# Optimization experiments

Hardware: AMD Instinct MI355X
Metric: run time of the kernel (lower is better)

Reference implementation:

```python
import jax, jax.numpy as jnp
import numpy as np
from math import factorial

# ---- static config (mirrors init_kwargs) ----
ZS = np.array([1, 6, 7, 8], dtype=np.int64)
NZ = 4
N_ATOM_BASIS = 3
CHAN = N_ATOM_BASIS ** 2          # 9 edge channels
MAX_L = 3
N_RBF = 8                          # radial basis functions
N_RB = 8                           # radial embedding dim
CUTOFF = 5.5
P_CUT = 6
MP_NORM = 1.0 / 10.0 ** 0.5        # 1/sqrt(avg_num_neighbors)
NUM_MP = 1
N_NODES = 4000
N_EDGES = 48000

def _make_l_list(max_l):
    lst = []
    for l in range(max_l + 1):
        for lx in range(l, -1, -1):
            for ly in range(l - lx, -1, -1):
                lst.append((lx, ly, l - lx - ly))
    return lst

L_LIST = _make_l_list(MAX_L)       # 20 (lx,ly,lz) tuples
N_L = len(L_LIST)
L_OF = np.array([sum(t) for t in L_LIST], dtype=np.int32)
LX = np.array([t[0] for t in L_LIST])
LY = np.array([t[1] for t in L_LIST])
LZ = np.array([t[2] for t in L_LIST])
# multinomial prefactors l!/(lx!ly!lz!), grouped per l for the nu=2 symmetrizer
PREF = np.array([factorial(sum(t)) / (factorial(t[0]) * factorial(t[1]) * factorial(t[2])) for t in L_LIST], dtype=np.float32)
SYM2 = np.zeros((N_L, MAX_L + 1), dtype=np.float32)
SYM2[np.arange(N_L), L_OF] = PREF

def _bessel_rbf(r):
    # r: [E,1] -> [E, N_RBF];  e_n(r) = sqrt(2/rc) * sin(n pi r / rc) / r
    n = jnp.arange(1, N_RBF + 1, dtype=r.dtype)
    return jnp.sqrt(2.0 / CUTOFF) * jnp.sin(n * jnp.pi * r / CUTOFF) / r

def _poly_cutoff(r):
    p = float(P_CUT)
    u = r / CUTOFF
    f = 1.0 - 0.5 * (p + 1.0) * (p + 2.0) * u ** p + p * (p + 2.0) * u ** (p + 1.0) - 0.5 * p * (p + 1.0) * u ** (p + 2.0)
    return f * (u < 1.0)

def _angular(unit):
    # monomials x^lx * y^ly * z^lz of the unit edge vector -> [E, N_L]
    x, y, z = unit[:, 0:1], unit[:, 1:2], unit[:, 2:3]
    return (x ** jnp.asarray(LX)) * (y ** jnp.asarray(LY)) * (z ** jnp.asarray(LZ))

def _radial_transform(A, W_rt):
    # shared per-l linear map along radial axis: [N, N_RBF, N_L, C] -> [N, N_RB, N_L, C]
    Wg = W_rt[jnp.asarray(L_OF)]   # [N_L, N_RBF, N_RB]
    return jnp.einsum('nric,irs->nsic', A, Wg)

def _symmetrize(A):
    # nu=1: A at lxlylz=(0,0,0); nu=2, each l: sum_{|lxlylz|=l} multinomial * A^2
    B1 = A[:, :, 0:1, :]
    B2 = jnp.einsum('nric,il->nrlc', A * A, jnp.asarray(SYM2))
    return jnp.concatenate([B1, B2], axis=2)   # [N, N_RB, 1+(MAX_L+1), C]

def _forward(positions, shifts, W_emb, W_rt, W_nm, atomic_numbers, edge_index):
    sender, receiver = edge_index[0], edge_index[1]
    one_hot = (atomic_numbers[:, None] == jnp.asarray(ZS)[None, :]).astype(positions.dtype)
    node_emb = one_hot @ W_emb                                    # [N, n_atom_basis]
    # edge encoding: flattened outer product of sender/receiver embeddings -> [E, CHAN]
    enc = (node_emb[sender][:, :, None] * node_emb[receiver][:, None, :]).reshape(-1, CHAN)
    vec = positions[receiver] - positions[sender] + shifts
    lengths = jnp.linalg.norm(vec, axis=-1, keepdims=True)        # [E,1]
    unit = vec / lengths
    rc = _bessel_rbf(lengths) * _poly_cutoff(lengths)             # [E, N_RBF]
    ang = _angular(unit)                                          # [E, N_L]
    edge_attri = rc[:, :, None, None] * ang[:, None, :, None] * enc[:, None, None, :]
    A = jax.ops.segment_sum(edge_attri, receiver, num_segments=N_NODES)
    A = _radial_transform(A, W_rt)                                # [N, N_RB, N_L, C]
    B = _symmetrize(A)
    feats = [B]
    Wnm_exp = W_nm[:, :, jnp.asarray(L_OF), :]                    # expand per-l memory weights to lxlylz
    for _ in range(NUM_MP):
        memory = A * Wnm_exp                                      # NodeMemory
        chi = B.sum(axis=(1, 2))                                  # [N, C] invariant scalar per channel
        msg_B = edge_attri * chi[sender][:, None, None, :]        # MesssageBchi
        A_B = _radial_transform(jax.ops.segment_sum(msg_B, receiver, num_segments=N_NODES), W_rt)
        msg_A = A[sender] * rc[:, :, None, None]                  # MessageAr: radial-weighted sender A
        A = (A_B + jax.ops.segment_sum(msg_A, receiver, num_segments=N_NODES)) * MP_NORM + memory
        B = _symmetrize(A)
        feats.append(B)
    return jnp.stack(feats, axis=-1)                              # [N, N_RB, 5, C, 1+NUM_MP]

def setup_inputs() -> dict:
    key = jax.random.key(0)
    k = jax.random.split(key, 8)
    positions = jax.random.uniform(k[0], (N_NODES, 3), dtype=jnp.float32) * 3.0
    shifts = jnp.zeros((N_EDGES, 3), dtype=jnp.float32)
    species_idx = jax.random.randint(k[1], (N_NODES,), 0, NZ)
    atomic_numbers = jnp.asarray(ZS)[species_idx]
    sender = jax.random.randint(k[2], (N_EDGES,), 0, N_NODES)
    receiver = (sender + 1 + jax.random.randint(k[3], (N_EDGES,), 0, N_NODES - 1)) % N_NODES  # no self-edges
    edge_index = jnp.stack([sender, receiver])
    W_emb = jax.random.normal(k[4], (NZ, N_ATOM_BASIS), dtype=jnp.float32) * 0.5
    W_rt = jax.random.normal(k[5], (MAX_L + 1, N_RBF, N_RB), dtype=jnp.float32) / np.sqrt(N_RBF)
    W_nm = jax.random.uniform(k[6], (1, N_RB, MAX_L + 1, CHAN), dtype=jnp.float32)
    return {"positions": positions, "shifts": shifts, "W_emb": W_emb, "W_rt": W_rt, "W_nm": W_nm, "atomic_numbers": atomic_numbers, "edge_index": edge_index}

def reference(positions, shifts, W_emb, W_rt, W_nm, atomic_numbers, edge_index):
    return _forward(positions, shifts, W_emb, W_rt, W_nm, atomic_numbers, edge_index)
```

## Files before the change

### kernel.cpp

```cpp
#include <hip/hip_runtime.h>
#include <hip/hip_fp16.h>

#ifndef M_PIf
#define M_PIf 3.14159265358979323846f
#endif

constexpr int NNODE = 4000;
constexpr int NEDGE = 48000;
constexpr int NLA   = 20;
constexpr int NCH   = 9;
constexpr int NRB   = 8;
constexpr int NEL   = NRB * NLA * NCH;
constexpr int NP2   = NEL / 2;
constexpr int FW    = 40;
constexpr int EC    = 32;
constexpr float CUT = 5.5f;
constexpr float MPN = 0.316227766016837933f;

__constant__ int   c_LOF[NLA]  = {0,1,1,1,2,2,2,2,2,2,3,3,3,3,3,3,3,3,3,3};
__constant__ float c_PREF[NLA] = {1,1,1,1,1,2,2,1,2,1,1,3,3,3,6,3,1,3,3,1};
__constant__ int   c_GB[4] = {0,0,1,4};
__constant__ int   c_GE[4] = {0,1,4,10};

__global__ void k_count(const int* __restrict__ ei, int* __restrict__ counts) {
  int e = blockIdx.x * blockDim.x + threadIdx.x;
  if (e >= NEDGE) return;
  atomicAdd(&counts[ei[NEDGE + e]], 1);
}

__global__ void k_scan(const int* __restrict__ counts, int* __restrict__ offsets,
                       int* __restrict__ cursor) {
  __shared__ int wsum[16];
  int t = threadIdx.x;
  int base = t*4;
  int c0 = (base+0 < NNODE) ? counts[base+0] : 0;
  int c1 = (base+1 < NNODE) ? counts[base+1] : 0;
  int c2 = (base+2 < NNODE) ? counts[base+2] : 0;
  int c3 = (base+3 < NNODE) ? counts[base+3] : 0;
  int s = c0+c1+c2+c3;
  int lane = t & 63, w = t >> 6;
  int incl = s;
  #pragma unroll
  for (int d = 1; d < 64; d <<= 1) {
    int v = __shfl_up(incl, d);
    if (lane >= d) incl += v;
  }
  if (lane == 63) wsum[w] = incl;
  __syncthreads();
  if (t < 16) {
    int v = wsum[t];
    int inc2 = v;
    #pragma unroll
    for (int d = 1; d < 16; d <<= 1) {
      int u = __shfl_up(inc2, d);
      if (t >= d) inc2 += u;
    }
    wsum[t] = inc2 - v;
  }
  __syncthreads();
  int excl = wsum[w] + incl - s;
  int o0 = excl, o1 = o0+c0, o2 = o1+c1, o3 = o2+c2;
  if (base+0 < NNODE) { offsets[base+0]=o0; cursor[base+0]=o0; }
  if (base+1 < NNODE) { offsets[base+1]=o1; cursor[base+1]=o1; }
  if (base+2 < NNODE) { offsets[base+2]=o2; cursor[base+2]=o2; }
  if (base+3 < NNODE) { offsets[base+3]=o3; cursor[base+3]=o3; }
  if (t == 1023) offsets[NNODE] = excl + s;
}

__global__ void k_edgec(const float* __restrict__ pos, const float* __restrict__ shifts,
                        const int* __restrict__ ei, const int* __restrict__ an,
                        const float* __restrict__ W_emb,
                        int* __restrict__ cursor, float* __restrict__ facS,
                        int* __restrict__ sndS) {
  int e = blockIdx.x * blockDim.x + threadIdx.x;
  if (e >= NEDGE) return;
  int snd = ei[e];
  int rcv = ei[NEDGE + e];
  float vx = pos[rcv*3+0] - pos[snd*3+0] + shifts[e*3+0];
  float vy = pos[rcv*3+1] - pos[snd*3+1] + shifts[e*3+1];
  float vz = pos[rcv*3+2] - pos[snd*3+2] + shifts[e*3+2];
  float len = sqrtf(vx*vx + vy*vy + vz*vz);
  float inv = 1.0f / len;
  float x = vx*inv, y = vy*inv, z = vz*inv;
  float u  = len * (1.0f/CUT);
  float u2 = u*u;
  float u6 = u2*u2*u2;
  float fcut = 1.0f - 28.0f*u6 + 48.0f*u6*u - 21.0f*u6*u2;
  if (u >= 1.0f) fcut = 0.0f;
  float pre = sqrtf(2.0f/CUT) * fcut * inv;
  int p = atomicAdd(&cursor[rcv], 1);
  float* f = facS + (size_t)p*FW;
  float s1 = __sinf(M_PIf * u);
  float cth = __cosf(M_PIf * u);
  float two_c = 2.0f * cth;
  float sm1 = 0.0f, sc = s1;
  #pragma unroll
  for (int j = 0; j < NRB; ++j) {
    f[j] = pre * sc;
    float nx = two_c * sc - sm1;
    sm1 = sc; sc = nx;
  }
  float ang[NLA];
  ang[0]=1.0f; ang[1]=x; ang[2]=y; ang[3]=z;
  ang[4]=x*x; ang[5]=x*y; ang[6]=x*z; ang[7]=y*y; ang[8]=y*z; ang[9]=z*z;
  ang[10]=ang[4]*x; ang[11]=ang[4]*y; ang[12]=ang[4]*z;
  ang[13]=x*ang[7]; ang[14]=ang[5]*z; ang[15]=x*ang[9];
  ang[16]=ang[7]*y; ang[17]=ang[7]*z; ang[18]=y*ang[9]; ang[19]=ang[9]*z;
  #pragma unroll
  for (int i = 0; i < NLA; ++i) f[8+i] = ang[i];
  int as_ = an[snd], ar_ = an[rcv];
  int sps = (as_==1)?0:(as_==6)?1:(as_==7)?2:3;
  int spr = (ar_==1)?0:(ar_==6)?1:(ar_==7)?2:3;
  float es0=W_emb[sps*3+0], es1=W_emb[sps*3+1], es2=W_emb[sps*3+2];
  float er0=W_emb[spr*3+0], er1=W_emb[spr*3+1], er2=W_emb[spr*3+2];
  f[28]=es0*er0; f[29]=es0*er1; f[30]=es0*er2;
  f[31]=es1*er0; f[32]=es1*er1; f[33]=es1*er2;
  f[34]=es2*er0; f[35]=es2*er1; f[36]=es2*er2;
  f[37]=0.f; f[38]=0.f; f[39]=0.f;
  sndS[p] = snd;
}

__global__ void k_echi(float* __restrict__ facS, const int* __restrict__ sndS,
                       const float* __restrict__ chi) {
  int p = blockIdx.x * blockDim.x + threadIdx.x;
  if (p >= NEDGE) return;
  int snd = sndS[p];
  float* f = facS + (size_t)p*FW;
  #pragma unroll
  for (int c = 0; c < 9; ++c)
    f[28 + c] = chi[snd*9 + c] * f[28 + c];
}


__global__ __launch_bounds__(256, 8) void k_nodeA(
    const float* __restrict__ facS, const int* __restrict__ offsets,
    const float* __restrict__ W_rt,
    __half2* __restrict__ A1h2,
    float* __restrict__ chi) {
  __shared__ float s_wrt[256];
  __shared__ float s_e[EC*FW];
  __shared__ float s_tile[8*90];
  __shared__ float s_B[288];
  int bid = blockIdx.x;
  int n = bid >> 1, half = bid & 1;
  int t = threadIdx.x;
  s_wrt[t] = W_rt[t];
  int rq[2], kk[2], i0[2], c0[2], l0[2], i1[2], c1[2], l1[2], qg[2];
  bool val[2];
  #pragma unroll
  for (int jj = 0; jj < 2; ++jj) {
    int j = t + jj*256;
    val[jj] = (j < 360);
    int js = val[jj] ? j : 0;
    rq[jj] = js / 45; kk[jj] = js % 45;
    qg[jj] = half*360 + js;
    int rem0 = 2*(kk[jj] + 45*half);
    i0[jj] = rem0 / 9;  c0[jj] = rem0 % 9;  l0[jj] = c_LOF[i0[jj]];
    int rem1 = rem0 + 1;
    i1[jj] = rem1 / 9;  c1[jj] = rem1 % 9;  l1[jj] = c_LOF[i1[jj]];
  }
  float acc[2][2] = {{0,0},{0,0}};
  int beg = offsets[n], end = offsets[n+1];
  const float4* f4 = (const float4*)facS;
  for (int base = beg; base < end; base += EC) {
    int m = min(EC, end - base);
    if (base != beg) __syncthreads();
    for (int idx = t; idx < m*(FW/4); idx += 256)
      ((float4*)s_e)[idx] = f4[(size_t)base*(FW/4) + idx];
    __syncthreads();
    for (int p = 0; p < m; ++p) {
      const float* e0 = s_e + p*FW;
      #pragma unroll
      for (int jj = 0; jj < 2; ++jj) {
        if (val[jj]) {
          float rv = e0[rq[jj]];
          acc[jj][0] += rv * e0[8+i0[jj]] * e0[28+c0[jj]];
          acc[jj][1] += rv * e0[8+i1[jj]] * e0[28+c1[jj]];
        }
      }
    }
  }
  __syncthreads();
  #pragma unroll
  for (int jj = 0; jj < 2; ++jj)
    if (val[jj]) {
      s_tile[rq[jj]*90 + 2*kk[jj]]     = acc[jj][0];
      s_tile[rq[jj]*90 + 2*kk[jj] + 1] = acc[jj][1];
    }
  __syncthreads();
  float a1v[2][2];
  #pragma unroll
  for (int jj = 0; jj < 2; ++jj) {
    if (val[jj]) {
      float ab0 = 0.f, ab1 = 0.f;
      #pragma unroll
      for (int r = 0; r < NRB; ++r) {
        ab0 += s_tile[r*90 + 2*kk[jj]]     * s_wrt[l0[jj]*64 + r*8 + rq[jj]];
        ab1 += s_tile[r*90 + 2*kk[jj] + 1] * s_wrt[l1[jj]*64 + r*8 + rq[jj]];
      }
      a1v[jj][0] = ab0; a1v[jj][1] = ab1;
      A1h2[(size_t)n*NP2 + qg[jj]] = __floats2half2_rn(ab0, ab1);
    }
  }
  __syncthreads();
  #pragma unroll
  for (int jj = 0; jj < 2; ++jj)
    if (val[jj]) {
      s_tile[rq[jj]*90 + 2*kk[jj]]     = a1v[jj][0];
      s_tile[rq[jj]*90 + 2*kk[jj] + 1] = a1v[jj][1];
    }
  __syncthreads();
  if (half == 0) {
    for (int m2 = t; m2 < 288; m2 += 256) {
      int s = m2 / 36, rm = m2 % 36, l5 = rm / 9, c = rm % 9;
      float b;
      if (l5 == 0) b = s_tile[s*90 + c];
      else {
        b = 0.f;
        for (int i = c_GB[l5]; i < c_GE[l5]; ++i) {
          float v = s_tile[s*90 + i*9 + c];
          b += c_PREF[i]*v*v;
        }
      }
      s_B[m2] = b;
    }
    __syncthreads();
    if (t < 9) {
      float x = 0.f;
      #pragma unroll
      for (int u = 0; u < 32; ++u) x += s_B[u*9 + t];
      atomicAdd(&chi[n*9 + t], x);
    }
  } else {
    if (t < 72) {
      int s = t / 9, c = t % 9;
      float b = 0.f;
      for (int i = 10; i < 20; ++i) {
        float v = s_tile[s*90 + (i-10)*9 + c];
        b += c_PREF[i]*v*v;
      }
      s_B[t] = b;
    }
    __syncthreads();
    if (t < 9) {
      float x = 0.f;
      #pragma unroll
      for (int u = 0; u < 8; ++u) x += s_B[u*9 + t];
      atomicAdd(&chi[n*9 + t], x);
    }
  }
}

__global__ __launch_bounds__(256, 8) void k_nodeMP(
    const float* __restrict__ facS, const int* __restrict__ offsets,
    const int* __restrict__ sndS,
    const float* __restrict__ W_rt, const float* __restrict__ W_nm,
    const __half2* __restrict__ A1h2,
    float* __restrict__ out) {
  __shared__ float s_wrt[256];
  __shared__ float s_wnm[288];
  __shared__ float s_e[EC*FW];
  __shared__ float s_tile[8*90];
  int bid = blockIdx.x;
  int n = bid >> 1, half = bid & 1;
  int t = threadIdx.x;
  s_wrt[t] = W_rt[t];
  s_wnm[t] = W_nm[t];
  if (t < 32) s_wnm[256 + t] = W_nm[256 + t];
  int rq[2], kk[2], i0[2], c0[2], l0[2], i1[2], c1[2], l1[2], qg[2];
  bool val[2];
  #pragma unroll
  for (int jj = 0; jj < 2; ++jj) {
    int j = t + jj*256;
    val[jj] = (j < 360);
    int js = val[jj] ? j : 0;
    rq[jj] = js / 45; kk[jj] = js % 45;
    qg[jj] = half*360 + js;
    int rem0 = 2*(kk[jj] + 45*half);
    i0[jj] = rem0 / 9;  c0[jj] = rem0 % 9;  l0[jj] = c_LOF[i0[jj]];
    int rem1 = rem0 + 1;
    i1[jj] = rem1 / 9;  c1[jj] = rem1 % 9;  l1[jj] = c_LOF[i1[jj]];
  }
  float accA[2][2] = {{0,0},{0,0}};
  float accB[2][2] = {{0,0},{0,0}};
  float2 mymem[2];
  #pragma unroll
  for (int jj = 0; jj < 2; ++jj)
    mymem[jj] = val[jj] ? __half22float2(A1h2[(size_t)n*NP2 + qg[jj]])
                        : make_float2(0.f, 0.f);
  int beg = offsets[n], end = offsets[n+1];
  const float4* f4 = (const float4*)facS;
  for (int base = beg; base < end; base += EC) {
    int m = min(EC, end - base);
    if (base != beg) __syncthreads();
    for (int idx = t; idx < m*(FW/4); idx += 256)
      ((float4*)s_e)[idx] = f4[(size_t)base*(FW/4) + idx];
    __syncthreads();
    int p = 0;
    for (; p + 3 < m; p += 4) {
      int sd0 = sndS[base+p+0], sd1 = sndS[base+p+1];
      int sd2 = sndS[base+p+2], sd3 = sndS[base+p+3];
      __half2 g0a = A1h2[(size_t)sd0*NP2 + qg[0]];
      __half2 g1a = A1h2[(size_t)sd1*NP2 + qg[0]];
      __half2 g2a = A1h2[(size_t)sd2*NP2 + qg[0]];
      __half2 g3a = A1h2[(size_t)sd3*NP2 + qg[0]];
      __half2 g0b, g1b, g2b, g3b;
      if (val[1]) {
        g0b = A1h2[(size_t)sd0*NP2 + qg[1]];
        g1b = A1h2[(size_t)sd1*NP2 + qg[1]];
        g2b = A1h2[(size_t)sd2*NP2 + qg[1]];
        g3b = A1h2[(size_t)sd3*NP2 + qg[1]];
      }
      #pragma unroll
      for (int x = 0; x < 4; ++x) {
        const float* e0 = s_e + (p+x)*FW;
        const float* x0 = e0 + 28;
        __half2 ga = (x==0)?g0a:(x==1)?g1a:(x==2)?g2a:g3a;
        {
          float rv = e0[rq[0]];
          float2 gf = __half22float2(ga);
          accA[0][0] += gf.x * rv;
          accA[0][1] += gf.y * rv;
          accB[0][0] += rv * e0[8+i0[0]] * x0[c0[0]];
          accB[0][1] += rv * e0[8+i1[0]] * x0[c1[0]];
        }
        if (val[1]) {
          __half2 gb = (x==0)?g0b:(x==1)?g1b:(x==2)?g2b:g3b;
          float rv = e0[rq[1]];
          float2 gf = __half22float2(gb);
          accA[1][0] += gf.x * rv;
          accA[1][1] += gf.y * rv;
          accB[1][0] += rv * e0[8+i0[1]] * x0[c0[1]];
          accB[1][1] += rv * e0[8+i1[1]] * x0[c1[1]];
        }
      }
    }
    for (; p < m; ++p) {
      int sd = sndS[base+p];
      const float* e0 = s_e + p*FW;
      const float* x0 = e0 + 28;
      const __half2* Ah = A1h2 + (size_t)sd*NP2;
      #pragma unroll
      for (int jj = 0; jj < 2; ++jj) {
        if (val[jj]) {
          float rv = e0[rq[jj]];
          float2 gf = __half22float2(Ah[qg[jj]]);
          accA[jj][0] += gf.x * rv;
          accA[jj][1] += gf.y * rv;
          accB[jj][0] += rv * e0[8+i0[jj]] * x0[c0[jj]];
          accB[jj][1] += rv * e0[8+i1[jj]] * x0[c1[jj]];
        }
      }
    }
  }
  __syncthreads();
  float* s_a1 = s_e;
  #pragma unroll
  for (int jj = 0; jj < 2; ++jj)
    if (val[jj]) {
      s_tile[rq[jj]*90 + 2*kk[jj]]     = accB[jj][0];
      s_tile[rq[jj]*90 + 2*kk[jj] + 1] = accB[jj][1];
      s_a1[rq[jj]*90 + 2*kk[jj]]       = mymem[jj].x;
      s_a1[rq[jj]*90 + 2*kk[jj] + 1]   = mymem[jj].y;
    }
  __syncthreads();
  float a2v[2][2];
  #pragma unroll
  for (int jj = 0; jj < 2; ++jj) {
    if (val[jj]) {
      float ab0 = 0.f, ab1 = 0.f;
      #pragma unroll
      for (int r = 0; r < NRB; ++r) {
        ab0 += s_tile[r*90 + 2*kk[jj]]     * s_wrt[l0[jj]*64 + r*8 + rq[jj]];
        ab1 += s_tile[r*90 + 2*kk[jj] + 1] * s_wrt[l1[jj]*64 + r*8 + rq[jj]];
      }
      float mem0 = mymem[jj].x * s_wnm[rq[jj]*36 + l0[jj]*9 + c0[jj]];
      float mem1 = mymem[jj].y * s_wnm[rq[jj]*36 + l1[jj]*9 + c1[jj]];
      a2v[jj][0] = (ab0 + accA[jj][0])*MPN + mem0;
      a2v[jj][1] = (ab1 + accA[jj][1])*MPN + mem1;
    }
  }
  __syncthreads();
  #pragma unroll
  for (int jj = 0; jj < 2; ++jj)
    if (val[jj]) {
      s_tile[rq[jj]*90 + 2*kk[jj]]     = a2v[jj][0];
      s_tile[rq[jj]*90 + 2*kk[jj] + 1] = a2v[jj][1];
    }
  __syncthreads();
  float2* o2 = (float2*)out;
  if (half == 0) {
    for (int m2 = t; m2 < 288; m2 += 256) {
      int s = m2 / 36, rm = m2 % 36, l5 = rm / 9, c = rm % 9;
      float b0, b1;
      if (l5 == 0) {
        b0 = s_a1[s*90 + c];
        b1 = s_tile[s*90 + c];
      } else {
        b0 = 0.f; b1 = 0.f;
        for (int i = c_GB[l5]; i < c_GE[l5]; ++i) {
          float v0 = s_a1[s*90 + i*9 + c];
          float v1 = s_tile[s*90 + i*9 + c];
          b0 += c_PREF[i]*v0*v0;
          b1 += c_PREF[i]*v1*v1;
        }
      }
      o2[(size_t)((n*8 + s)*5 + l5)*9 + c] = make_float2(b0, b1);
    }
  } else {
    if (t < 72) {
      int s = t / 9, c = t % 9;
      float b0 = 0.f, b1 = 0.f;
      for (int i = 10; i < 20; ++i) {
        float v0 = s_a1[s*90 + (i-10)*9 + c];
        float v1 = s_tile[s*90 + (i-10)*9 + c];
        b0 += c_PREF[i]*v0*v0;
        b1 += c_PREF[i]*v1*v1;
      }
      o2[(size_t)((n*8 + s)*5 + 4)*9 + c] = make_float2(b0, b1);
    }
  }
}

extern "C" void kernel_launch(void* const* d_in, const int* in_sizes, int n_in,
                              void* d_out, int out_size, void* d_ws, size_t ws_size,
                              hipStream_t stream) {
  const float* pos    = (const float*)d_in[0];
  const float* shifts = (const float*)d_in[1];
  const float* W_emb  = (const float*)d_in[2];
  const float* W_rt   = (const float*)d_in[3];
  const float* W_nm   = (const float*)d_in[4];
  const int*   an     = (const int*)d_in[5];
  const int*   ei     = (const int*)d_in[6];
  float* out = (float*)d_out;

  char* ws = (char*)d_ws;
  size_t off = 0;
  auto carve = [&](size_t bytes) {
    void* p = ws + off;
    off = (off + bytes + 255) & ~(size_t)255;
    return p;
  };
  float*   facS    = (float*)carve((size_t)FW*NEDGE*sizeof(float));
  int*     sndS    = (int*)carve((size_t)NEDGE*sizeof(int));
  __half2* A1h2    = (__half2*)carve((size_t)NNODE*NEL*sizeof(__half));
  float*   chi     = (float*)carve((size_t)NNODE*NCH*sizeof(float));
  int*     counts  = (int*)carve((size_t)NNODE*sizeof(int));
  int*     offsets = (int*)carve((size_t)(NNODE+1)*sizeof(int));
  int*     cursor  = (int*)carve((size_t)NNODE*sizeof(int));

  size_t z0 = (size_t)((char*)chi - ws);
  size_t z1 = (size_t)((char*)counts - ws) + (size_t)NNODE*sizeof(int);
  hipMemsetAsync((char*)ws + z0, 0, z1 - z0, stream);
  k_count<<<(NEDGE+255)/256, 256, 0, stream>>>(ei, counts);
  k_scan<<<1, 1024, 0, stream>>>(counts, offsets, cursor);
  k_edgec<<<(NEDGE+255)/256, 256, 0, stream>>>(pos, shifts, ei, an, W_emb, cursor, facS, sndS);
  k_nodeA<<<NNODE*2, 256, 0, stream>>>(facS, offsets, W_rt, A1h2, chi);
  k_echi<<<(NEDGE+255)/256, 256, 0, stream>>>(facS, sndS, chi);
  k_nodeMP<<<NNODE*2, 256, 0, stream>>>(facS, offsets, sndS, W_rt, W_nm, A1h2, out);
}
```

Before: 112.5 us.

## Process each node with one block instead of two half-blocks

Both node kernels now use one 256-thread block per node covering all 720 half2 pairs, with three pairs per thread, instead of two blocks each covering half the pairs. Each node's edge tile is loaded once instead of twice, and chi is written directly rather than accumulated with atomics, so the chi region no longer needs a memset. In exchange the grid has half as many blocks, each thread holds more registers (k_nodeMP launch bounds drop to 6 blocks per SM), and threads past the 720th pair sit idle on the third slot.

```diff
diff --git a/kernel.cpp b/kernel.cpp
--- a/kernel.cpp
+++ b/kernel.cpp
@@ -19,8 +19,8 @@
 
 __constant__ int   c_LOF[NLA]  = {0,1,1,1,2,2,2,2,2,2,3,3,3,3,3,3,3,3,3,3};
 __constant__ float c_PREF[NLA] = {1,1,1,1,1,2,2,1,2,1,1,3,3,3,6,3,1,3,3,1};
-__constant__ int   c_GB[4] = {0,0,1,4};
-__constant__ int   c_GE[4] = {0,1,4,10};
+__constant__ int   c_GB[5] = {0,0,1,4,10};
+__constant__ int   c_GE[5] = {0,1,4,10,20};
 
 __global__ void k_count(const int* __restrict__ ei, int* __restrict__ counts) {
   int e = blockIdx.x * blockDim.x + threadIdx.x;
@@ -139,27 +139,26 @@
     float* __restrict__ chi) {
   __shared__ float s_wrt[256];
   __shared__ float s_e[EC*FW];
-  __shared__ float s_tile[8*90];
-  __shared__ float s_B[288];
-  int bid = blockIdx.x;
-  int n = bid >> 1, half = bid & 1;
+  __shared__ float s_tile[NEL];
+  __shared__ float s_B[360];
+  int n = blockIdx.x;
   int t = threadIdx.x;
   s_wrt[t] = W_rt[t];
-  int rq[2], kk[2], i0[2], c0[2], l0[2], i1[2], c1[2], l1[2], qg[2];
-  bool val[2];
-  #pragma unroll
-  for (int jj = 0; jj < 2; ++jj) {
-    int j = t + jj*256;
-    val[jj] = (j < 360);
-    int js = val[jj] ? j : 0;
-    rq[jj] = js / 45; kk[jj] = js % 45;
-    qg[jj] = half*360 + js;
-    int rem0 = 2*(kk[jj] + 45*half);
-    i0[jj] = rem0 / 9;  c0[jj] = rem0 % 9;  l0[jj] = c_LOF[i0[jj]];
-    int rem1 = rem0 + 1;
-    i1[jj] = rem1 / 9;  c1[jj] = rem1 % 9;  l1[jj] = c_LOF[i1[jj]];
-  }
-  float acc[2][2] = {{0,0},{0,0}};
+  int qq[3], rq[3], rem0[3], i0[3], c0[3], l0[3], i1[3], c1[3], l1[3];
+  bool val[3];
+  #pragma unroll
+  for (int jj = 0; jj < 3; ++jj) {
+    int q = t + jj*256;
+    val[jj] = (q < NP2);
+    int qs = val[jj] ? q : 0;
+    qq[jj] = qs;
+    rq[jj] = qs / 90;
+    rem0[jj] = (2*qs) % 180;
+    i0[jj] = rem0[jj] / 9;  c0[jj] = rem0[jj] % 9;  l0[jj] = c_LOF[i0[jj]];
+    int r1 = rem0[jj] + 1;
+    i1[jj] = r1 / 9;  c1[jj] = r1 % 9;  l1[jj] = c_LOF[i1[jj]];
+  }
+  float acc[3][2] = {{0,0},{0,0},{0,0}};
   int beg = offsets[n], end = offsets[n+1];
   const float4* f4 = (const float4*)facS;
   for (int base = beg; base < end; base += EC) {
@@ -171,7 +170,7 @@
     for (int p = 0; p < m; ++p) {
       const float* e0 = s_e + p*FW;
       #pragma unroll
-      for (int jj = 0; jj < 2; ++jj) {
+      for (int jj = 0; jj < 3; ++jj) {
         if (val[jj]) {
           float rv = e0[rq[jj]];
           acc[jj][0] += rv * e0[8+i0[jj]] * e0[28+c0[jj]];
@@ -182,76 +181,57 @@
   }
   __syncthreads();
   #pragma unroll
-  for (int jj = 0; jj < 2; ++jj)
-    if (val[jj]) {
-      s_tile[rq[jj]*90 + 2*kk[jj]]     = acc[jj][0];
-      s_tile[rq[jj]*90 + 2*kk[jj] + 1] = acc[jj][1];
-    }
-  __syncthreads();
-  float a1v[2][2];
-  #pragma unroll
-  for (int jj = 0; jj < 2; ++jj) {
+  for (int jj = 0; jj < 3; ++jj)
+    if (val[jj]) {
+      s_tile[rq[jj]*180 + rem0[jj]]     = acc[jj][0];
+      s_tile[rq[jj]*180 + rem0[jj] + 1] = acc[jj][1];
+    }
+  __syncthreads();
+  float a1v[3][2];
+  #pragma unroll
+  for (int jj = 0; jj < 3; ++jj) {
     if (val[jj]) {
       float ab0 = 0.f, ab1 = 0.f;
       #pragma unroll
       for (int r = 0; r < NRB; ++r) {
-        ab0 += s_tile[r*90 + 2*kk[jj]]     * s_wrt[l0[jj]*64 + r*8 + rq[jj]];
-        ab1 += s_tile[r*90 + 2*kk[jj] + 1] * s_wrt[l1[jj]*64 + r*8 + rq[jj]];
+        ab0 += s_tile[r*180 + rem0[jj]]     * s_wrt[l0[jj]*64 + r*8 + rq[jj]];
+        ab1 += s_tile[r*180 + rem0[jj] + 1] * s_wrt[l1[jj]*64 + r*8 + rq[jj]];
       }
       a1v[jj][0] = ab0; a1v[jj][1] = ab1;
-      A1h2[(size_t)n*NP2 + qg[jj]] = __floats2half2_rn(ab0, ab1);
-    }
-  }
-  __syncthreads();
-  #pragma unroll
-  for (int jj = 0; jj < 2; ++jj)
-    if (val[jj]) {
-      s_tile[rq[jj]*90 + 2*kk[jj]]     = a1v[jj][0];
-      s_tile[rq[jj]*90 + 2*kk[jj] + 1] = a1v[jj][1];
-    }
-  __syncthreads();
-  if (half == 0) {
-    for (int m2 = t; m2 < 288; m2 += 256) {
-      int s = m2 / 36, rm = m2 % 36, l5 = rm / 9, c = rm % 9;
-      float b;
-      if (l5 == 0) b = s_tile[s*90 + c];
-      else {
-        b = 0.f;
-        for (int i = c_GB[l5]; i < c_GE[l5]; ++i) {
-          float v = s_tile[s*90 + i*9 + c];
-          b += c_PREF[i]*v*v;
-        }
-      }
-      s_B[m2] = b;
-    }
-    __syncthreads();
-    if (t < 9) {
-      float x = 0.f;
-      #pragma unroll
-      for (int u = 0; u < 32; ++u) x += s_B[u*9 + t];
-      atomicAdd(&chi[n*9 + t], x);
-    }
-  } else {
-    if (t < 72) {
-      int s = t / 9, c = t % 9;
-      float b = 0.f;
-      for (int i = 10; i < 20; ++i) {
-        float v = s_tile[s*90 + (i-10)*9 + c];
+      A1h2[(size_t)n*NP2 + qq[jj]] = __floats2half2_rn(ab0, ab1);
+    }
+  }
+  __syncthreads();
+  #pragma unroll
+  for (int jj = 0; jj < 3; ++jj)
+    if (val[jj]) {
+      s_tile[rq[jj]*180 + rem0[jj]]     = a1v[jj][0];
+      s_tile[rq[jj]*180 + rem0[jj] + 1] = a1v[jj][1];
+    }
+  __syncthreads();
+  for (int m2 = t; m2 < 360; m2 += 256) {
+    int s = m2 / 45, rm = m2 % 45, l5 = rm / 9, c = rm % 9;
+    float b;
+    if (l5 == 0) b = s_tile[s*180 + c];
+    else {
+      b = 0.f;
+      for (int i = c_GB[l5]; i < c_GE[l5]; ++i) {
+        float v = s_tile[s*180 + i*9 + c];
         b += c_PREF[i]*v*v;
       }
-      s_B[t] = b;
-    }
-    __syncthreads();
-    if (t < 9) {
-      float x = 0.f;
-      #pragma unroll
-      for (int u = 0; u < 8; ++u) x += s_B[u*9 + t];
-      atomicAdd(&chi[n*9 + t], x);
-    }
-  }
-}
-
-__global__ __launch_bounds__(256, 8) void k_nodeMP(
+    }
+    s_B[m2] = b;
+  }
+  __syncthreads();
+  if (t < 9) {
+    float x = 0.f;
+    #pragma unroll
+    for (int u = 0; u < 40; ++u) x += s_B[u*9 + t];
+    chi[n*9 + t] = x;
+  }
+}
+
+__global__ __launch_bounds__(256, 6) void k_nodeMP(
     const float* __restrict__ facS, const int* __restrict__ offsets,
     const int* __restrict__ sndS,
     const float* __restrict__ W_rt, const float* __restrict__ W_nm,
@@ -259,34 +239,33 @@
     float* __restrict__ out) {
   __shared__ float s_wrt[256];
   __shared__ float s_wnm[288];
-  __shared__ float s_e[EC*FW];
-  __shared__ float s_tile[8*90];
-  int bid = blockIdx.x;
-  int n = bid >> 1, half = bid & 1;
+  __shared__ float s_e[NEL];
+  __shared__ float s_tile[NEL];
+  int n = blockIdx.x;
   int t = threadIdx.x;
   s_wrt[t] = W_rt[t];
   s_wnm[t] = W_nm[t];
   if (t < 32) s_wnm[256 + t] = W_nm[256 + t];
-  int rq[2], kk[2], i0[2], c0[2], l0[2], i1[2], c1[2], l1[2], qg[2];
-  bool val[2];
-  #pragma unroll
-  for (int jj = 0; jj < 2; ++jj) {
-    int j = t + jj*256;
-    val[jj] = (j < 360);
-    int js = val[jj] ? j : 0;
-    rq[jj] = js / 45; kk[jj] = js % 45;
-    qg[jj] = half*360 + js;
-    int rem0 = 2*(kk[jj] + 45*half);
-    i0[jj] = rem0 / 9;  c0[jj] = rem0 % 9;  l0[jj] = c_LOF[i0[jj]];
-    int rem1 = rem0 + 1;
-    i1[jj] = rem1 / 9;  c1[jj] = rem1 % 9;  l1[jj] = c_LOF[i1[jj]];
-  }
-  float accA[2][2] = {{0,0},{0,0}};
-  float accB[2][2] = {{0,0},{0,0}};
-  float2 mymem[2];
-  #pragma unroll
-  for (int jj = 0; jj < 2; ++jj)
-    mymem[jj] = val[jj] ? __half22float2(A1h2[(size_t)n*NP2 + qg[jj]])
+  int qq[3], rq[3], rem0[3], i0[3], c0[3], l0[3], i1[3], c1[3], l1[3];
+  bool val[3];
+  #pragma unroll
+  for (int jj = 0; jj < 3; ++jj) {
+    int q = t + jj*256;
+    val[jj] = (q < NP2);
+    int qs = val[jj] ? q : 0;
+    qq[jj] = qs;
+    rq[jj] = qs / 90;
+    rem0[jj] = (2*qs) % 180;
+    i0[jj] = rem0[jj] / 9;  c0[jj] = rem0[jj] % 9;  l0[jj] = c_LOF[i0[jj]];
+    int r1 = rem0[jj] + 1;
+    i1[jj] = r1 / 9;  c1[jj] = r1 % 9;  l1[jj] = c_LOF[i1[jj]];
+  }
+  float accA[3][2] = {{0,0},{0,0},{0,0}};
+  float accB[3][2] = {{0,0},{0,0},{0,0}};
+  float2 mymem[3];
+  #pragma unroll
+  for (int jj = 0; jj < 3; ++jj)
+    mymem[jj] = val[jj] ? __half22float2(A1h2[(size_t)n*NP2 + qq[jj]])
                         : make_float2(0.f, 0.f);
   int beg = offsets[n], end = offsets[n+1];
   const float4* f4 = (const float4*)facS;
@@ -300,22 +279,22 @@
     for (; p + 3 < m; p += 4) {
       int sd0 = sndS[base+p+0], sd1 = sndS[base+p+1];
       int sd2 = sndS[base+p+2], sd3 = sndS[base+p+3];
-      __half2 g0a = A1h2[(size_t)sd0*NP2 + qg[0]];
-      __half2 g1a = A1h2[(size_t)sd1*NP2 + qg[0]];
-      __half2 g2a = A1h2[(size_t)sd2*NP2 + qg[0]];
-      __half2 g3a = A1h2[(size_t)sd3*NP2 + qg[0]];
-      __half2 g0b, g1b, g2b, g3b;
-      if (val[1]) {
-        g0b = A1h2[(size_t)sd0*NP2 + qg[1]];
-        g1b = A1h2[(size_t)sd1*NP2 + qg[1]];
-        g2b = A1h2[(size_t)sd2*NP2 + qg[1]];
-        g3b = A1h2[(size_t)sd3*NP2 + qg[1]];
+      const __half2* A0 = A1h2 + (size_t)sd0*NP2;
+      const __half2* A1 = A1h2 + (size_t)sd1*NP2;
+      const __half2* A2 = A1h2 + (size_t)sd2*NP2;
+      const __half2* A3 = A1h2 + (size_t)sd3*NP2;
+      __half2 g0a = A0[qq[0]], g1a = A1[qq[0]], g2a = A2[qq[0]], g3a = A3[qq[0]];
+      __half2 g0b = A0[qq[1]], g1b = A1[qq[1]], g2b = A2[qq[1]], g3b = A3[qq[1]];
+      __half2 g0c, g1c, g2c, g3c;
+      if (val[2]) {
+        g0c = A0[qq[2]]; g1c = A1[qq[2]]; g2c = A2[qq[2]]; g3c = A3[qq[2]];
       }
       #pragma unroll
       for (int x = 0; x < 4; ++x) {
         const float* e0 = s_e + (p+x)*FW;
         const float* x0 = e0 + 28;
         __half2 ga = (x==0)?g0a:(x==1)?g1a:(x==2)?g2a:g3a;
+        __half2 gb = (x==0)?g0b:(x==1)?g1b:(x==2)?g2b:g3b;
         {
           float rv = e0[rq[0]];
           float2 gf = __half22float2(ga);
@@ -324,8 +303,7 @@
           accB[0][0] += rv * e0[8+i0[0]] * x0[c0[0]];
           accB[0][1] += rv * e0[8+i1[0]] * x0[c1[0]];
         }
-        if (val[1]) {
-          __half2 gb = (x==0)?g0b:(x==1)?g1b:(x==2)?g2b:g3b;
+        {
           float rv = e0[rq[1]];
           float2 gf = __half22float2(gb);
           accA[1][0] += gf.x * rv;
@@ -333,6 +311,15 @@
           accB[1][0] += rv * e0[8+i0[1]] * x0[c0[1]];
           accB[1][1] += rv * e0[8+i1[1]] * x0[c1[1]];
         }
+        if (val[2]) {
+          __half2 gc = (x==0)?g0c:(x==1)?g1c:(x==2)?g2c:g3c;
+          float rv = e0[rq[2]];
+          float2 gf = __half22float2(gc);
+          accA[2][0] += gf.x * rv;
+          accA[2][1] += gf.y * rv;
+          accB[2][0] += rv * e0[8+i0[2]] * x0[c0[2]];
+          accB[2][1] += rv * e0[8+i1[2]] * x0[c1[2]];
+        }
       }
     }
     for (; p < m; ++p) {
@@ -341,10 +328,10 @@
       const float* x0 = e0 + 28;
       const __half2* Ah = A1h2 + (size_t)sd*NP2;
       #pragma unroll
-      for (int jj = 0; jj < 2; ++jj) {
+      for (int jj = 0; jj < 3; ++jj) {
         if (val[jj]) {
           float rv = e0[rq[jj]];
-          float2 gf = __half22float2(Ah[qg[jj]]);
+          float2 gf = __half22float2(Ah[qq[jj]]);
           accA[jj][0] += gf.x * rv;
           accA[jj][1] += gf.y * rv;
           accB[jj][0] += rv * e0[8+i0[jj]] * x0[c0[jj]];
@@ -356,23 +343,23 @@
   __syncthreads();
   float* s_a1 = s_e;
   #pragma unroll
-  for (int jj = 0; jj < 2; ++jj)
-    if (val[jj]) {
-      s_tile[rq[jj]*90 + 2*kk[jj]]     = accB[jj][0];
-      s_tile[rq[jj]*90 + 2*kk[jj] + 1] = accB[jj][1];
-      s_a1[rq[jj]*90 + 2*kk[jj]]       = mymem[jj].x;
-      s_a1[rq[jj]*90 + 2*kk[jj] + 1]   = mymem[jj].y;
-    }
-  __syncthreads();
-  float a2v[2][2];
-  #pragma unroll
-  for (int jj = 0; jj < 2; ++jj) {
+  for (int jj = 0; jj < 3; ++jj)
+    if (val[jj]) {
+      s_tile[rq[jj]*180 + rem0[jj]]     = accB[jj][0];
+      s_tile[rq[jj]*180 + rem0[jj] + 1] = accB[jj][1];
+      s_a1[rq[jj]*180 + rem0[jj]]       = mymem[jj].x;
+      s_a1[rq[jj]*180 + rem0[jj] + 1]   = mymem[jj].y;
+    }
+  __syncthreads();
+  float a2v[3][2];
+  #pragma unroll
+  for (int jj = 0; jj < 3; ++jj) {
     if (val[jj]) {
       float ab0 = 0.f, ab1 = 0.f;
       #pragma unroll
       for (int r = 0; r < NRB; ++r) {
-        ab0 += s_tile[r*90 + 2*kk[jj]]     * s_wrt[l0[jj]*64 + r*8 + rq[jj]];
-        ab1 += s_tile[r*90 + 2*kk[jj] + 1] * s_wrt[l1[jj]*64 + r*8 + rq[jj]];
+        ab0 += s_tile[r*180 + rem0[jj]]     * s_wrt[l0[jj]*64 + r*8 + rq[jj]];
+        ab1 += s_tile[r*180 + rem0[jj] + 1] * s_wrt[l1[jj]*64 + r*8 + rq[jj]];
       }
       float mem0 = mymem[jj].x * s_wnm[rq[jj]*36 + l0[jj]*9 + c0[jj]];
       float mem1 = mymem[jj].y * s_wnm[rq[jj]*36 + l1[jj]*9 + c1[jj]];
@@ -382,43 +369,29 @@
   }
   __syncthreads();
   #pragma unroll
-  for (int jj = 0; jj < 2; ++jj)
-    if (val[jj]) {
-      s_tile[rq[jj]*90 + 2*kk[jj]]     = a2v[jj][0];
-      s_tile[rq[jj]*90 + 2*kk[jj] + 1] = a2v[jj][1];
+  for (int jj = 0; jj < 3; ++jj)
+    if (val[jj]) {
+      s_tile[rq[jj]*180 + rem0[jj]]     = a2v[jj][0];
+      s_tile[rq[jj]*180 + rem0[jj] + 1] = a2v[jj][1];
     }
   __syncthreads();
   float2* o2 = (float2*)out;
-  if (half == 0) {
-    for (int m2 = t; m2 < 288; m2 += 256) {
-      int s = m2 / 36, rm = m2 % 36, l5 = rm / 9, c = rm % 9;
-      float b0, b1;
-      if (l5 == 0) {
-        b0 = s_a1[s*90 + c];
-        b1 = s_tile[s*90 + c];
-      } else {
-        b0 = 0.f; b1 = 0.f;
-        for (int i = c_GB[l5]; i < c_GE[l5]; ++i) {
-          float v0 = s_a1[s*90 + i*9 + c];
-          float v1 = s_tile[s*90 + i*9 + c];
-          b0 += c_PREF[i]*v0*v0;
-          b1 += c_PREF[i]*v1*v1;
-        }
-      }
-      o2[(size_t)((n*8 + s)*5 + l5)*9 + c] = make_float2(b0, b1);
-    }
-  } else {
-    if (t < 72) {
-      int s = t / 9, c = t % 9;
-      float b0 = 0.f, b1 = 0.f;
-      for (int i = 10; i < 20; ++i) {
-        float v0 = s_a1[s*90 + (i-10)*9 + c];
-        float v1 = s_tile[s*90 + (i-10)*9 + c];
+  for (int m2 = t; m2 < 360; m2 += 256) {
+    int s = m2 / 45, rm = m2 % 45, l5 = rm / 9, c = rm % 9;
+    float b0, b1;
+    if (l5 == 0) {
+      b0 = s_a1[s*180 + c];
+      b1 = s_tile[s*180 + c];
+    } else {
+      b0 = 0.f; b1 = 0.f;
+      for (int i = c_GB[l5]; i < c_GE[l5]; ++i) {
+        float v0 = s_a1[s*180 + i*9 + c];
+        float v1 = s_tile[s*180 + i*9 + c];
         b0 += c_PREF[i]*v0*v0;
         b1 += c_PREF[i]*v1*v1;
       }
-      o2[(size_t)((n*8 + s)*5 + 4)*9 + c] = make_float2(b0, b1);
-    }
+    }
+    o2[(size_t)n*360 + m2] = make_float2(b0, b1);
   }
 }
 
@@ -449,13 +422,11 @@
   int*     offsets = (int*)carve((size_t)(NNODE+1)*sizeof(int));
   int*     cursor  = (int*)carve((size_t)NNODE*sizeof(int));
 
-  size_t z0 = (size_t)((char*)chi - ws);
-  size_t z1 = (size_t)((char*)counts - ws) + (size_t)NNODE*sizeof(int);
-  hipMemsetAsync((char*)ws + z0, 0, z1 - z0, stream);
+  hipMemsetAsync(counts, 0, (size_t)NNODE*sizeof(int), stream);
   k_count<<<(NEDGE+255)/256, 256, 0, stream>>>(ei, counts);
   k_scan<<<1, 1024, 0, stream>>>(counts, offsets, cursor);
   k_edgec<<<(NEDGE+255)/256, 256, 0, stream>>>(pos, shifts, ei, an, W_emb, cursor, facS, sndS);
-  k_nodeA<<<NNODE*2, 256, 0, stream>>>(facS, offsets, W_rt, A1h2, chi);
+  k_nodeA<<<NNODE, 256, 0, stream>>>(facS, offsets, W_rt, A1h2, chi);
   k_echi<<<(NEDGE+255)/256, 256, 0, stream>>>(facS, sndS, chi);
-  k_nodeMP<<<NNODE*2, 256, 0, stream>>>(facS, offsets, sndS, W_rt, W_nm, A1h2, out);
-}
+  k_nodeMP<<<NNODE, 256, 0, stream>>>(facS, offsets, sndS, W_rt, W_nm, A1h2, out);
+}
```

New measurement: 117.1 us. +4.0%, slower.
